# Performance work log

Hardware: AMD Instinct MI355X
Metric: run time of the kernel (lower is better)

Reference implementation:

```python
import jax, jax.numpy as jnp
import numpy as np

D_EMB = 1024
B, T = 8, 2048

def setup_inputs() -> dict:
    key = jax.random.key(0)
    ks = jax.random.split(key, 7)
    s = 0.02
    return {
        "x": jax.random.normal(ks[0], (B, T, D_EMB), dtype=jnp.float32),
        "W_attn": jax.random.normal(ks[1], (3 * D_EMB, D_EMB), dtype=jnp.float32) * s,
        "b_attn": jax.random.normal(ks[2], (3 * D_EMB,), dtype=jnp.float32) * s,
        "W_proj": jax.random.normal(ks[3], (D_EMB, D_EMB), dtype=jnp.float32) * s,
        "b_proj": jax.random.normal(ks[4], (D_EMB,), dtype=jnp.float32) * s,
        "W_fc": jax.random.normal(ks[5], (1, D_EMB), dtype=jnp.float32) * s,
        "b_fc": jax.random.normal(ks[6], (1,), dtype=jnp.float32) * s,
    }

def reference(x, W_attn, b_attn, W_proj, b_proj, W_fc, b_fc):
    # qkv projection: torch Linear => x @ W.T + b
    qkv = jnp.einsum('btc,dc->btd', x, W_attn) + b_attn          # [B,T,3C]
    q, k, v = jnp.split(qkv, 3, axis=2)                          # each [B,T,C]
    scale = q.shape[-1] ** (-0.5)
    attn_scores = jnp.einsum('btc,bsc->bts', q, k) * scale       # [B,T,T]
    attn_weights = jax.nn.softmax(attn_scores, axis=-1)          # traditional softmax
    y = jnp.einsum('bts,bsc->btc', attn_weights, v)              # [B,T,C]
    y = jnp.einsum('btc,dc->btd', y, W_proj) + b_proj            # [B,T,C]
    out = jnp.einsum('btc,oc->bto', y, W_fc) + b_fc              # [B,T,1]
    return out
```

## Files before the change

### kernel.cpp

```cpp
#include <hip/hip_runtime.h>
#include <stdint.h>

#define D_EMB 1024
#define NBATCH 8
#define SEQ 2048
#define MTOT (NBATCH*SEQ)

typedef __attribute__((ext_vector_type(8))) short short8;
typedef __attribute__((ext_vector_type(4))) float f32x4;

__device__ __forceinline__ ushort bf16r(float x) {
  union { float f; uint32_t u; } c; c.f = x;
  return (ushort)((c.u + 0x7fffu + ((c.u >> 16) & 1u)) >> 16);
}

__device__ __forceinline__ void cp16(const ushort* g, ushort* l) {
  __builtin_amdgcn_global_load_lds(
      (const __attribute__((address_space(1))) void*)g,
      (__attribute__((address_space(3))) void*)l, 16, 0, 0);
}

__global__ __launch_bounds__(256) void cvt_all(
    const float4* __restrict__ x4, const float4* __restrict__ W4,
    const float4* __restrict__ wv4, const float* __restrict__ sc,
    ushort* __restrict__ xb, ushort* __restrict__ wqkb, float* __restrict__ vw) {
  int tid = threadIdx.x;
  if (blockIdx.x < 4096) {
    int wave = tid >> 6, lane = tid & 63;
    long row = (long)blockIdx.x * 4 + wave;
    const float4* xr = x4 + row * 256;
    ushort* xo = xb + row * D_EMB;
    float s = 0.f;
    #pragma unroll
    for (int i = 0; i < 4; i++) {
      int idx = lane + i * 64;
      float4 v = xr[idx];
      float4 w = wv4[idx];
      *(ushort4*)(xo + idx * 4) = make_ushort4(bf16r(v.x), bf16r(v.y), bf16r(v.z), bf16r(v.w));
      s += v.x * w.x + v.y * w.y + v.z * w.z + v.w * w.w;
    }
    #pragma unroll
    for (int off = 32; off; off >>= 1) s += __shfl_xor(s, off);
    if (lane == 0) vw[row] = s + sc[1];
  } else {
    long base = (long)(blockIdx.x - 4096) * 1024 + tid;
    #pragma unroll
    for (int i = 0; i < 4; i++) {
      long idx = base + i * 256;
      float4 v = W4[idx];
      *(ushort4*)(wqkb + idx * 4) = make_ushort4(bf16r(v.x), bf16r(v.y), bf16r(v.z), bf16r(v.w));
    }
  }
}

__global__ void init_kernel(const float* __restrict__ bp, const float* __restrict__ Wfc,
                            const float* __restrict__ bfc,
                            float* __restrict__ w_eff, float* __restrict__ wv_eff,
                            float* __restrict__ numden, float* __restrict__ sc) {
  int tid = threadIdx.x;
  int b = blockIdx.x;
  if (b == 0) { w_eff[tid] = 0.f; return; }
  if (b == 1) { wv_eff[tid] = 0.f; return; }
  if (b >= 3) { numden[(long)(b - 3) * 1024 + tid] = 0.f; return; }
  float v = bp[tid] * Wfc[tid];
  int lane = tid & 63, w = tid >> 6;
  #pragma unroll
  for (int off = 32; off; off >>= 1) v += __shfl_xor(v, off);
  __shared__ float red[16];
  if (lane == 0) red[w] = v;
  __syncthreads();
  if (tid == 0) {
    float s = 0.f;
    #pragma unroll
    for (int i = 0; i < 16; i++) s += red[i];
    sc[0] = s + bfc[0];
  }
}

__global__ void prep1(const float* __restrict__ Wp, const float* __restrict__ Wfc,
                      float* __restrict__ w_eff) {
  int c = blockIdx.x * 256 + threadIdx.x;
  int d0 = blockIdx.y * 16;
  float s = 0.f;
  #pragma unroll
  for (int d = d0; d < d0 + 16; d++) s += Wfc[d] * Wp[(long)d * D_EMB + c];
  atomicAdd(&w_eff[c], s);
}

__global__ void prep2(const float* __restrict__ Wattn, const float* __restrict__ battn,
                      const float* __restrict__ w_eff, float* __restrict__ wv_eff,
                      float* __restrict__ sc) {
  int tid = threadIdx.x;
  if (blockIdx.y == 64) {
    if (blockIdx.x != 0) return;
    float v = 0.f;
    #pragma unroll
    for (int i = 0; i < 4; i++) { int c = tid + i * 256; v += battn[2048 + c] * w_eff[c]; }
    int lane = tid & 63, w = tid >> 6;
    #pragma unroll
    for (int off = 32; off; off >>= 1) v += __shfl_xor(v, off);
    __shared__ float red[4];
    if (lane == 0) red[w] = v;
    __syncthreads();
    if (tid == 0) sc[1] = red[0] + red[1] + red[2] + red[3];
    return;
  }
  int d = blockIdx.x * 256 + tid;
  int c0 = blockIdx.y * 16;
  float s = 0.f;
  #pragma unroll
  for (int c = c0; c < c0 + 16; c++) s += w_eff[c] * Wattn[(long)(2048 + c) * D_EMB + d];
  atomicAdd(&wv_eff[d], s);
}

template<bool FUSED, bool REMAP>
__global__ __launch_bounds__(512, 2) void gemm_nt(
    const ushort* __restrict__ A, long lda, long sAz,
    const ushort* __restrict__ B, long ldb, long sBz,
    ushort* __restrict__ C, long ldc,
    const float* __restrict__ bias, float scale, int K,
    const float* __restrict__ vw, float* __restrict__ num, float* __restrict__ den) {
  __shared__ __align__(16) ushort lds[65536];

  int bx, by, z;
  if (REMAP) {
    int f = (int)(blockIdx.x + 8u * blockIdx.y);
    int xcd = f & 7, g = f >> 3;
    bx = g & 7; by = xcd * 8 + (g >> 3); z = 0;
  } else {
    bx = blockIdx.x; by = blockIdx.y; z = blockIdx.z;
  }

  const ushort* Az = A + (long)z * sAz;
  const ushort* Bz = B + (long)z * sBz;
  long m0 = (long)by * 256, n0 = (long)bx * 256;
  int t = threadIdx.x;
  int wave = t >> 6, lane = t & 63;
  int r = lane & 15, q = lane >> 4;
  int wm = wave >> 2, wn = wave & 3;

  f32x4 acc[8][4] = {};

  int srow0 = t >> 2, srow1 = srow0 + 128;
  int scs = t & 3;
  const ushort* pA0 = Az + (m0 + srow0) * lda + (long)((scs ^ ((srow0 >> 1) & 3)) * 8);
  const ushort* pA1 = Az + (m0 + srow1) * lda + (long)((scs ^ ((srow1 >> 1) & 3)) * 8);
  const ushort* pB0 = Bz + (n0 + srow0) * ldb + (long)((scs ^ ((srow0 >> 1) & 3)) * 8);
  const ushort* pB1 = Bz + (n0 + srow1) * ldb + (long)((scs ^ ((srow1 >> 1) & 3)) * 8);
  ushort* ldsA = lds;
  ushort* ldsB = lds + 32768;
  int d0 = t * 8, d1 = (t + 512) * 8;

  int swz8 = (q ^ ((r >> 1) & 3)) * 8;
  int offa = (wm * 128 + r) * 32 + swz8;
  int offb = (wn * 64 + r) * 32 + swz8;

  int NT = K >> 6;
  int SMAX = 2 * NT;

#define STAGE(tile_, kk_) do { \
    long ko_ = (long)(tile_) * 64 + (long)(kk_) * 32; \
    int rg_ = (((tile_) & 1) * 2 + (kk_)) * 8192; \
    cp16(pA0 + ko_, ldsA + rg_ + d0); \
    cp16(pA1 + ko_, ldsA + rg_ + d1); \
    cp16(pB0 + ko_, ldsB + rg_ + d0); \
    cp16(pB1 + ko_, ldsB + rg_ + d1); \
  } while (0)

#define VM8 asm volatile("s_waitcnt vmcnt(8)" ::: "memory")
#define VM4 asm volatile("s_waitcnt vmcnt(4)" ::: "memory")
#define VM0 asm volatile("s_waitcnt vmcnt(0)" ::: "memory")
#define VMNONE (void)0

#define PHASE(RG, DOSTAGE, ST_, SK_, WAITOP) do { \
    if (DOSTAGE) STAGE(ST_, SK_); \
    short8 af[8], bfr[4]; \
    _Pragma("unroll") \
    for (int fr = 0; fr < 8; fr++) \
      af[fr] = *(const short8*)(ldsA + (RG) * 8192 + offa + fr * 512); \
    _Pragma("unroll") \
    for (int j = 0; j < 4; j++) \
      bfr[j] = *(const short8*)(ldsB + (RG) * 8192 + offb + j * 512); \
    __builtin_amdgcn_s_barrier(); \
    asm volatile("s_waitcnt lgkmcnt(0)" ::: "memory"); \
    __builtin_amdgcn_s_setprio(1); \
    _Pragma("unroll") \
    for (int fr = 0; fr < 8; fr++) { \
      _Pragma("unroll") \
      for (int j = 0; j < 4; j++) \
        acc[fr][j] = __builtin_amdgcn_mfma_f32_16x16x32_bf16(af[fr], bfr[j], acc[fr][j], 0, 0, 0); \
    } \
    __builtin_amdgcn_s_setprio(0); \
    WAITOP; \
    __builtin_amdgcn_s_barrier(); \
  } while (0)

  STAGE(0, 0); STAGE(0, 1); STAGE(1, 0);
  VM8;
  __builtin_amdgcn_s_barrier();

  for (int s = 0; s < SMAX - 4; s += 4) {
    PHASE(0, true, (s + 3) >> 1, (s + 3) & 1, VM8);
    PHASE(1, true, (s + 4) >> 1, (s + 4) & 1, VM8);
    PHASE(2, true, (s + 5) >> 1, (s + 5) & 1, VM8);
    PHASE(3, true, (s + 6) >> 1, (s + 6) & 1, VM8);
  }
  PHASE(0, true,  NT - 1, 1, VM8);
  PHASE(1, false, 0, 0, VM4);
  PHASE(2, false, 0, 0, VM0);
  PHASE(3, false, 0, 0, VMNONE);
#undef PHASE
#undef STAGE

  if (!FUSED) {
    #pragma unroll
    for (int fr = 0; fr < 8; fr++) {
      #pragma unroll
      for (int j = 0; j < 4; j++) {
        long col = n0 + wn * 64 + j * 16 + r;
        float bj = bias[col];
        #pragma unroll
        for (int rr = 0; rr < 4; rr++) {
          long row = m0 + wm * 128 + fr * 16 + q * 4 + rr;
          C[row * ldc + col] = bf16r(acc[fr][j][rr] * scale + bj);
        }
      }
    }
  } else {
    const float* vwz = vw + (long)z * SEQ + n0;
    float* numz = num + (long)z * SEQ + m0;
    float* denz = den + (long)z * SEQ + m0;
    float vwj[4];
    #pragma unroll
    for (int j = 0; j < 4; j++) vwj[j] = vwz[wn * 64 + j * 16 + r];
    #pragma unroll
    for (int fr = 0; fr < 8; fr++) {
      #pragma unroll
      for (int rr = 0; rr < 4; rr++) {
        float sn = 0.f, sd = 0.f;
        #pragma unroll
        for (int j = 0; j < 4; j++) {
          float e = __expf(acc[fr][j][rr] * scale);
          sd += e;
          sn += e * vwj[j];
        }
        #pragma unroll
        for (int off = 1; off < 16; off <<= 1) {
          sn += __shfl_xor(sn, off);
          sd += __shfl_xor(sd, off);
        }
        if (r == 0) {
          int row = wm * 128 + fr * 16 + q * 4 + rr;
          atomicAdd(&numz[row], sn);
          atomicAdd(&denz[row], sd);
        }
      }
    }
  }
}

__global__ __launch_bounds__(256) void finalize(
    const float* __restrict__ num, const float* __restrict__ den,
    const float* __restrict__ sc, float* __restrict__ out) {
  long i = blockIdx.x * 256L + threadIdx.x;
  out[i] = num[i] / den[i] + sc[0];
}

extern "C" void kernel_launch(void* const* d_in, const int* in_sizes, int n_in,
                              void* d_out, int out_size, void* d_ws, size_t ws_size,
                              hipStream_t stream) {
  const float* x     = (const float*)d_in[0];
  const float* Wattn = (const float*)d_in[1];
  const float* battn = (const float*)d_in[2];
  const float* Wproj = (const float*)d_in[3];
  const float* bproj = (const float*)d_in[4];
  const float* Wfc   = (const float*)d_in[5];
  const float* bfc   = (const float*)d_in[6];
  float* out = (float*)d_out;

  const size_t OFF_XB    = 0;
  const size_t OFF_WQKB  = 33554432;
  const size_t OFF_QK    = 37748736;
  const size_t OFF_NUM   = 104857600;
  const size_t OFF_DEN   = 104923136;
  const size_t OFF_VW    = 104988672;
  const size_t OFF_WEFF  = 105054208;
  const size_t OFF_WVEFF = 105058304;
  const size_t OFF_SC    = 105062400;
  const size_t NEED      = 105062408;
  if (ws_size < NEED) return;

  char* ws = (char*)d_ws;
  ushort* xb    = (ushort*)(ws + OFF_XB);
  ushort* wqkb  = (ushort*)(ws + OFF_WQKB);
  ushort* qk    = (ushort*)(ws + OFF_QK);
  float* num    = (float*)(ws + OFF_NUM);
  float* den    = (float*)(ws + OFF_DEN);
  float* vw     = (float*)(ws + OFF_VW);
  float* w_eff  = (float*)(ws + OFF_WEFF);
  float* wv_eff = (float*)(ws + OFF_WVEFF);
  float* sc     = (float*)(ws + OFF_SC);

  init_kernel<<<dim3(35), dim3(1024), 0, stream>>>(bproj, Wfc, bfc, w_eff, wv_eff, num, sc);
  prep1<<<dim3(4, 64), dim3(256), 0, stream>>>(Wproj, Wfc, w_eff);
  prep2<<<dim3(4, 65), dim3(256), 0, stream>>>(Wattn, battn, w_eff, wv_eff, sc);

  cvt_all<<<dim3(4096 + 512), dim3(256), 0, stream>>>(
      (const float4*)x, (const float4*)Wattn, (const float4*)wv_eff, sc, xb, wqkb, vw);

  gemm_nt<false, true><<<dim3(8, 64, 1), dim3(512), 0, stream>>>(
      xb, (long)D_EMB, 0L, wqkb, (long)D_EMB, 0L,
      qk, 2048L, battn, 1.0f, D_EMB, nullptr, nullptr, nullptr);

  gemm_nt<true, false><<<dim3(8, 8, NBATCH), dim3(512), 0, stream>>>(
      qk, 2048L, (long)SEQ * 2048, qk + 1024, 2048L, (long)SEQ * 2048,
      nullptr, 0L, nullptr, 0.03125f, D_EMB, vw, num, den);

  finalize<<<dim3(64), dim3(256), 0, stream>>>(num, den, sc, out);
}
```

Before: 275.1 us.

## Restructure GEMM main loop into quadrant-split ping-pong pipeline with 64-wide K tiles

```diff
diff --git a/kernel.cpp b/kernel.cpp
--- a/kernel.cpp
+++ b/kernel.cpp
@@ -141,88 +141,119 @@
 
   f32x4 acc[8][4] = {};
 
-  int srow0 = t >> 2, srow1 = srow0 + 128;
-  int scs = t & 3;
-  const ushort* pA0 = Az + (m0 + srow0) * lda + (long)((scs ^ ((srow0 >> 1) & 3)) * 8);
-  const ushort* pA1 = Az + (m0 + srow1) * lda + (long)((scs ^ ((srow1 >> 1) & 3)) * 8);
-  const ushort* pB0 = Bz + (n0 + srow0) * ldb + (long)((scs ^ ((srow0 >> 1) & 3)) * 8);
-  const ushort* pB1 = Bz + (n0 + srow1) * ldb + (long)((scs ^ ((srow1 >> 1) & 3)) * 8);
-  ushort* ldsA = lds;
-  ushort* ldsB = lds + 32768;
-  int d0 = t * 8, d1 = (t + 512) * 8;
-
-  int swz8 = (q ^ ((r >> 1) & 3)) * 8;
-  int offa = (wm * 128 + r) * 32 + swz8;
-  int offb = (wn * 64 + r) * 32 + swz8;
+  int rl = t >> 3;
+  int cs = t & 7;
+  int gc = cs ^ (rl & 7);
+  const ushort* pA = Az + (m0 + rl) * lda + gc * 8;
+  const ushort* pB = Bz + (n0 + rl) * ldb + gc * 8;
+  long a64 = 64 * lda, a128 = 128 * lda;
+  long b64 = 64 * ldb, b128s = 128 * ldb;
+  int dst = t * 8;
+
+  int sw8 = (q ^ (r & 7)) * 8;
+  int aoff = (wm * 128 + r) * 64 + sw8;
+  int boff = (wn * 64 + r) * 64 + sw8;
 
   int NT = K >> 6;
-  int SMAX = 2 * NT;
-
-#define STAGE(tile_, kk_) do { \
-    long ko_ = (long)(tile_) * 64 + (long)(kk_) * 32; \
-    int rg_ = (((tile_) & 1) * 2 + (kk_)) * 8192; \
-    cp16(pA0 + ko_, ldsA + rg_ + d0); \
-    cp16(pA1 + ko_, ldsA + rg_ + d1); \
-    cp16(pB0 + ko_, ldsB + rg_ + d0); \
-    cp16(pB1 + ko_, ldsB + rg_ + d1); \
-  } while (0)
-
-#define VM8 asm volatile("s_waitcnt vmcnt(8)" ::: "memory")
+
+#define STG_A(BUF, H, TT) do { \
+    cp16(pA + (long)(TT) * 64 + (H) * a128,       lds + (BUF) * 16384 + (H) * 8192 + dst); \
+    cp16(pA + (long)(TT) * 64 + (H) * a128 + a64, lds + (BUF) * 16384 + (H) * 8192 + 4096 + dst); \
+  } while (0)
+#define STG_B(BUF, H, TT) do { \
+    cp16(pB + (long)(TT) * 64 + (H) * b128s,       lds + 32768 + (BUF) * 16384 + (H) * 8192 + dst); \
+    cp16(pB + (long)(TT) * 64 + (H) * b128s + b64, lds + 32768 + (BUF) * 16384 + (H) * 8192 + 4096 + dst); \
+  } while (0)
+
+#define LDA_Q(BUF, QA) do { \
+    _Pragma("unroll") \
+    for (int i = 0; i < 4; i++) { \
+      af[0][i] = *(const short8*)(lds + (BUF) * 16384 + ( aoff + (QA) * 4096 + i * 1024       )); \
+      af[1][i] = *(const short8*)(lds + (BUF) * 16384 + ((aoff + (QA) * 4096 + i * 1024) ^ 32 )); \
+    } \
+  } while (0)
+#define LDB_Q(BUF, QB, BF) do { \
+    _Pragma("unroll") \
+    for (int j = 0; j < 2; j++) { \
+      BF[0][j] = *(const short8*)(lds + 32768 + (BUF) * 16384 + ( boff + (QB) * 2048 + j * 1024       )); \
+      BF[1][j] = *(const short8*)(lds + 32768 + (BUF) * 16384 + ((boff + (QB) * 2048 + j * 1024) ^ 32 )); \
+    } \
+  } while (0)
+
+#define MM_Q(QA, QB, BF) do { \
+    __builtin_amdgcn_s_setprio(1); \
+    _Pragma("unroll") \
+    for (int kk = 0; kk < 2; kk++) { \
+      _Pragma("unroll") \
+      for (int i = 0; i < 4; i++) { \
+        _Pragma("unroll") \
+        for (int j = 0; j < 2; j++) \
+          acc[(QA) * 4 + i][(QB) * 2 + j] = __builtin_amdgcn_mfma_f32_16x16x32_bf16( \
+              af[kk][i], BF[kk][j], acc[(QA) * 4 + i][(QB) * 2 + j], 0, 0, 0); \
+      } \
+    } \
+    __builtin_amdgcn_s_setprio(0); \
+  } while (0)
+
+#define BAR __builtin_amdgcn_s_barrier()
+#define LGKM0 asm volatile("s_waitcnt lgkmcnt(0)" ::: "memory")
 #define VM4 asm volatile("s_waitcnt vmcnt(4)" ::: "memory")
 #define VM0 asm volatile("s_waitcnt vmcnt(0)" ::: "memory")
-#define VMNONE (void)0
-
-#define PHASE(RG, DOSTAGE, ST_, SK_, WAITOP) do { \
-    if (DOSTAGE) STAGE(ST_, SK_); \
-    short8 af[8], bfr[4]; \
-    _Pragma("unroll") \
-    for (int fr = 0; fr < 8; fr++) \
-      af[fr] = *(const short8*)(ldsA + (RG) * 8192 + offa + fr * 512); \
-    _Pragma("unroll") \
-    for (int j = 0; j < 4; j++) \
-      bfr[j] = *(const short8*)(ldsB + (RG) * 8192 + offb + j * 512); \
-    __builtin_amdgcn_s_barrier(); \
-    asm volatile("s_waitcnt lgkmcnt(0)" ::: "memory"); \
-    __builtin_amdgcn_s_setprio(1); \
-    _Pragma("unroll") \
-    for (int fr = 0; fr < 8; fr++) { \
-      _Pragma("unroll") \
-      for (int j = 0; j < 4; j++) \
-        acc[fr][j] = __builtin_amdgcn_mfma_f32_16x16x32_bf16(af[fr], bfr[j], acc[fr][j], 0, 0, 0); \
-    } \
-    __builtin_amdgcn_s_setprio(0); \
-    WAITOP; \
-    __builtin_amdgcn_s_barrier(); \
-  } while (0)
-
-  STAGE(0, 0); STAGE(0, 1); STAGE(1, 0);
-  VM8;
-  __builtin_amdgcn_s_barrier();
-
-  for (int s = 0; s < SMAX - 4; s += 4) {
-    PHASE(0, true, (s + 3) >> 1, (s + 3) & 1, VM8);
-    PHASE(1, true, (s + 4) >> 1, (s + 4) & 1, VM8);
-    PHASE(2, true, (s + 5) >> 1, (s + 5) & 1, VM8);
-    PHASE(3, true, (s + 6) >> 1, (s + 6) & 1, VM8);
-  }
-  PHASE(0, true,  NT - 1, 1, VM8);
-  PHASE(1, false, 0, 0, VM4);
-  PHASE(2, false, 0, 0, VM0);
-  PHASE(3, false, 0, 0, VMNONE);
-#undef PHASE
-#undef STAGE
+
+#define TILE(BUF, OB, TT, DOA, DOB, P4WAIT) do { \
+    short8 af[2][4], bf0[2][2], bf1[2][2]; \
+     \
+    LDA_Q(BUF, 0); LDB_Q(BUF, 0, bf0); \
+    if (DOA) STG_A(OB, 0, (TT) + 1); \
+    BAR; LGKM0; MM_Q(0, 0, bf0); BAR; \
+     \
+    LDB_Q(BUF, 1, bf1); \
+    if (DOA) STG_A(OB, 1, (TT) + 1); \
+    BAR; LGKM0; MM_Q(0, 1, bf1); BAR; \
+     \
+    LDA_Q(BUF, 1); \
+    if (DOB) STG_B(BUF, 0, (TT) + 2); \
+    BAR; LGKM0; MM_Q(1, 1, bf1); BAR; \
+     \
+    if (DOB) STG_B(BUF, 1, (TT) + 2); \
+    BAR; MM_Q(1, 0, bf0); P4WAIT; BAR; \
+  } while (0)
+
+  STG_A(0, 0, 0); STG_A(0, 1, 0); STG_B(0, 0, 0); STG_B(0, 1, 0);
+  STG_B(1, 0, 1); STG_B(1, 1, 1);
+  VM4;
+  BAR;
+
+  #pragma unroll 1
+  for (int u = 0; u < NT - 2; u += 2) {
+    TILE(0, 1, u,     true, true, VM4);
+    TILE(1, 0, u + 1, true, true, VM4);
+  }
+  TILE(0, 1, NT - 2, true,  false, VM0);
+  TILE(1, 0, NT - 1, false, false, (void)0);
+
+#undef TILE
+#undef BAR
+#undef LGKM0
+#undef VM4
+#undef VM0
+#undef MM_Q
+#undef LDB_Q
+#undef LDA_Q
+#undef STG_B
+#undef STG_A
 
   if (!FUSED) {
     #pragma unroll
-    for (int fr = 0; fr < 8; fr++) {
+    for (int fi = 0; fi < 8; fi++) {
       #pragma unroll
-      for (int j = 0; j < 4; j++) {
-        long col = n0 + wn * 64 + j * 16 + r;
+      for (int fj = 0; fj < 4; fj++) {
+        long col = n0 + wn * 64 + fj * 16 + r;
         float bj = bias[col];
         #pragma unroll
         for (int rr = 0; rr < 4; rr++) {
-          long row = m0 + wm * 128 + fr * 16 + q * 4 + rr;
-          C[row * ldc + col] = bf16r(acc[fr][j][rr] * scale + bj);
+          long row = m0 + wm * 128 + fi * 16 + q * 4 + rr;
+          C[row * ldc + col] = bf16r(acc[fi][fj][rr] * scale + bj);
         }
       }
     }
@@ -232,17 +263,17 @@
     float* denz = den + (long)z * SEQ + m0;
     float vwj[4];
     #pragma unroll
-    for (int j = 0; j < 4; j++) vwj[j] = vwz[wn * 64 + j * 16 + r];
-    #pragma unroll
-    for (int fr = 0; fr < 8; fr++) {
+    for (int fj = 0; fj < 4; fj++) vwj[fj] = vwz[wn * 64 + fj * 16 + r];
+    #pragma unroll
+    for (int fi = 0; fi < 8; fi++) {
       #pragma unroll
       for (int rr = 0; rr < 4; rr++) {
         float sn = 0.f, sd = 0.f;
         #pragma unroll
-        for (int j = 0; j < 4; j++) {
-          float e = __expf(acc[fr][j][rr] * scale);
+        for (int fj = 0; fj < 4; fj++) {
+          float e = __expf(acc[fi][fj][rr] * scale);
           sd += e;
-          sn += e * vwj[j];
+          sn += e * vwj[fj];
         }
         #pragma unroll
         for (int off = 1; off < 16; off <<= 1) {
@@ -250,7 +281,7 @@
           sd += __shfl_xor(sd, off);
         }
         if (r == 0) {
-          int row = wm * 128 + fr * 16 + q * 4 + rr;
+          int row = wm * 128 + fi * 16 + q * 4 + rr;
           atomicAdd(&numz[row], sn);
           atomicAdd(&denz[row], sd);
         }
```

Measured after the change: 276.2 us. About the same (+0.4%).
